# Kernel optimization log

Measured on AMD Instinct MI355X. Metric: run time of the kernel, lower is better.

Reference implementation:

```python
import jax, jax.numpy as jnp
import numpy as np
from jax import lax


def setup_inputs() -> dict:
    key = jax.random.key(0)
    k1, k2 = jax.random.split(key)
    x = jax.random.normal(k1, (16, 256, 64, 64), dtype=jnp.float32)
    weight = jax.random.normal(k2, (1024, 256), dtype=jnp.float32)  # codebook (K, C)
    return {"x": x, "weight": weight}


def reference(x, weight):
    B, C, H, W = x.shape
    # (b c h w) -> (b h w) c
    xf = jnp.transpose(x, (0, 2, 3, 1)).reshape(-1, C)  # [N, C]
    d = (jnp.sum(xf * xf, axis=1, keepdims=True)
         + jnp.sum(weight * weight, axis=1)
         - 2.0 * (xf @ weight.T))
    indices = jnp.argmin(d, axis=1)  # [N], int
    z = weight[indices]  # [N, C] embedding lookup
    codebook_loss = jnp.mean((z - lax.stop_gradient(xf)) ** 2)
    commitment_loss = jnp.mean((xf - lax.stop_gradient(z)) ** 2)
    # straight-through estimator
    zq = xf + lax.stop_gradient(z - xf)
    zq = zq.reshape(B, H, W, C).transpose(0, 3, 1, 2)  # back to [B, C, H, W]
    sequence = indices.reshape(B, H, W)
    return zq, sequence, codebook_loss, commitment_loss
```

## Files before the change

kernel.cpp:

```cpp
#include <hip/hip_runtime.h>
#include <cfloat>
#include <climits>

#define B_   16
#define C_   256
#define K_   1024
#define HW_  4096
#define N_   (B_ * HW_)
#define CHW_ (C_ * HW_)

#define SEQ_OFF  16777216
#define LOSS_OFF (SEQ_OFF + N_)
#define WT_F    0
#define WN_F    262144
#define WNU_F   263168
#define WQ_F    264192
#define RLIST_F 395264
#define RCNT_F  526336
#define WMAX_F  526337

#define RL_CAP  131072
#define EPS_GAP 0.1f
#define XSCL    20.0f
#define XINV    0.05f
#define XOVF    6.3f

typedef int i32x4 __attribute__((ext_vector_type(4)));

__device__ __forceinline__ int pack4b(int b0, int b1, int b2, int b3) {
    return (b0 & 0xFF) | ((b1 & 0xFF) << 8) | ((b2 & 0xFF) << 16) | ((b3 & 0xFF) << 24);
}

__global__ __launch_bounds__(256) void wmax_kernel(
    const float* __restrict__ w, unsigned* __restrict__ wmax_bits)
{
    const int tid = blockIdx.x * 256 + threadIdx.x;
    float mx = 0.f;
#pragma unroll
    for (int q = 0; q < 4; ++q) {
        const float4 v = reinterpret_cast<const float4*>(w)[tid * 4 + q];
        mx = fmaxf(mx, fmaxf(fmaxf(fabsf(v.x), fabsf(v.y)), fmaxf(fabsf(v.z), fabsf(v.w))));
    }
#pragma unroll
    for (int m = 1; m < 64; m <<= 1) mx = fmaxf(mx, __shfl_xor(mx, m, 64));
    if ((threadIdx.x & 63) == 0) atomicMax(wmax_bits, __float_as_uint(mx));
}

__global__ __launch_bounds__(256) void wprep_kernel(
    const float* __restrict__ w, const unsigned* __restrict__ wmax_bits,
    unsigned char* __restrict__ wq, float* __restrict__ w_t,
    float* __restrict__ wn, int* __restrict__ wnu)
{
    const int t = threadIdx.x;
    const int l = t & 63;
    const int k = blockIdx.x * 4 + (t >> 6);
    const float wmx = __uint_as_float(*wmax_bits);
    const float s   = 127.4f / wmx;
    const float d1  = wmx / 127.4f;
    const float sl  = s * 256.0f;

    const float4 v4 = *reinterpret_cast<const float4*>(w + (size_t)k * C_ + l * 4);
    float vv[4] = {v4.x, v4.y, v4.z, v4.w};
    float s2 = vv[0]*vv[0] + vv[1]*vv[1] + vv[2]*vv[2] + vv[3]*vv[3];
#pragma unroll
    for (int m = 1; m < 64; m <<= 1) s2 += __shfl_xor(s2, m, 64);

    const int chunk = k >> 4;
    const int col   = k & 15;
#pragma unroll
    for (int q = 0; q < 4; ++q) {
        const int c = l * 4 + q;
        const float v = vv[q];
        const int qh = (int)rintf(v * s);
        const float r = fmaf((float)qh, -d1, v);
        int ql = (int)rintf(r * sl);
        ql = max(-127, min(127, ql));
        const size_t off = (size_t)chunk * 8192 + (size_t)(c >> 6) * 1024
                         + (size_t)((c >> 4) & 3) * 256 + (size_t)col * 16 + (size_t)(c & 15);
        wq[off]        = (unsigned char)(qh & 0xFF);
        wq[off + 4096] = (unsigned char)(ql & 0xFF);
        w_t[(size_t)c * K_ + k] = v;
    }
    if (l == 0) {
        wn[k] = s2;
        wnu[k] = (int)rintf(s2 * (2560.0f / d1));
    }
}

__global__ __launch_bounds__(64, 2) void argmin_i8_kernel(
    const float* __restrict__ x, const unsigned char* __restrict__ wq,
    const int* __restrict__ wnu, const unsigned* __restrict__ wmax_bits,
    float* __restrict__ seq, int* __restrict__ rlist, int* __restrict__ rcount)
{
    const int l   = threadIdx.x;
    const int col = l & 15;
    const int kg  = l >> 4;
    const int nb  = blockIdx.x;
    const int b   = nb >> 7;
    const int hw0 = (nb & 127) << 5;
    const float* xb = x + (size_t)b * CHW_ + hw0;

    i32x4 ah[2][4], al[2][4];
    float mxr[2] = {0.f, 0.f};
#pragma unroll
    for (int t = 0; t < 2; ++t) {
        const int row = t * 16 + col;
#pragma unroll
        for (int s = 0; s < 4; ++s) {
            int qh[16], ql[16];
#pragma unroll
            for (int j = 0; j < 16; ++j) {
                const float v = xb[(size_t)(s * 64 + kg * 16 + j) * HW_ + row];
                mxr[t] = fmaxf(mxr[t], fabsf(v));
                int h = (int)rintf(v * XSCL);
                h = max(-127, min(127, h));
                const float r = fmaf((float)h, -XINV, v);
                int lo = (int)rintf(r * (XSCL * 256.0f));
                lo = max(-127, min(127, lo));
                qh[j] = h; ql[j] = lo;
            }
            ah[t][s] = (i32x4){ pack4b(qh[0],qh[1],qh[2],qh[3]),   pack4b(qh[4],qh[5],qh[6],qh[7]),
                                pack4b(qh[8],qh[9],qh[10],qh[11]), pack4b(qh[12],qh[13],qh[14],qh[15]) };
            al[t][s] = (i32x4){ pack4b(ql[0],ql[1],ql[2],ql[3]),   pack4b(ql[4],ql[5],ql[6],ql[7]),
                                pack4b(ql[8],ql[9],ql[10],ql[11]), pack4b(ql[12],ql[13],ql[14],ql[15]) };
        }
    }

#pragma unroll
    for (int t = 0; t < 2; ++t) {
        mxr[t] = fmaxf(mxr[t], __shfl_xor(mxr[t], 16, 64));
        mxr[t] = fmaxf(mxr[t], __shfl_xor(mxr[t], 32, 64));
        if (kg == 0 && mxr[t] > XOVF) {
            const int pos = atomicAdd(rcount, 1);
            if (pos < RL_CAP) rlist[pos] = b * HW_ + hw0 + t * 16 + col;
        }
    }

    const float wmx = __uint_as_float(*wmax_bits);
    const int eps_u = (int)(32614.4f / wmx);

    int m1p[2][4], m2p[2][4];
#pragma unroll
    for (int t = 0; t < 2; ++t)
#pragma unroll
        for (int i = 0; i < 4; ++i) { m1p[t][i] = INT_MAX; m2p[t][i] = INT_MAX; }

#pragma unroll 1
    for (int ch = 0; ch < 64; ++ch) {
        const unsigned char* base = wq + (size_t)ch * 8192 + l * 16;
        const int wnu_l = wnu[ch * 16 + col];

        i32x4 bh[4], bl[4];
#pragma unroll
        for (int s = 0; s < 4; ++s) {
            bh[s] = *reinterpret_cast<const i32x4*>(base + s * 1024);
            bl[s] = *reinterpret_cast<const i32x4*>(base + 4096 + s * 1024);
        }

        i32x4 aH0 = {0,0,0,0}, aH1 = {0,0,0,0};
        i32x4 aXa0 = {0,0,0,0}, aXb0 = {0,0,0,0};
        i32x4 aXa1 = {0,0,0,0}, aXb1 = {0,0,0,0};
#pragma unroll
        for (int s = 0; s < 4; ++s) {
            aH0  = __builtin_amdgcn_mfma_i32_16x16x64_i8(ah[0][s], bh[s], aH0, 0, 0, 0);
            aH1  = __builtin_amdgcn_mfma_i32_16x16x64_i8(ah[1][s], bh[s], aH1, 0, 0, 0);
            aXa0 = __builtin_amdgcn_mfma_i32_16x16x64_i8(ah[0][s], bl[s], aXa0, 0, 0, 0);
            aXb0 = __builtin_amdgcn_mfma_i32_16x16x64_i8(al[0][s], bh[s], aXb0, 0, 0, 0);
            aXa1 = __builtin_amdgcn_mfma_i32_16x16x64_i8(ah[1][s], bl[s], aXa1, 0, 0, 0);
            aXb1 = __builtin_amdgcn_mfma_i32_16x16x64_i8(al[1][s], bh[s], aXb1, 0, 0, 0);
        }

#pragma unroll
        for (int i = 0; i < 4; ++i) {
            const int T0  = (aH0[i] << 8) + aXa0[i] + aXb0[i];
            const int D0  = wnu_l - T0;
            const int Dp0 = (D0 & ~63) | ch;
            m2p[0][i] = min(m2p[0][i], max(m1p[0][i], Dp0));
            m1p[0][i] = min(m1p[0][i], Dp0);
            const int T1  = (aH1[i] << 8) + aXa1[i] + aXb1[i];
            const int D1  = wnu_l - T1;
            const int Dp1 = (D1 & ~63) | ch;
            m2p[1][i] = min(m2p[1][i], max(m1p[1][i], Dp1));
            m1p[1][i] = min(m1p[1][i], Dp1);
        }
    }

    int k1[2][4];
#pragma unroll
    for (int t = 0; t < 2; ++t)
#pragma unroll
        for (int i = 0; i < 4; ++i) k1[t][i] = ((m1p[t][i] & 63) << 4) | col;
#pragma unroll
    for (int mask = 1; mask <= 8; mask <<= 1) {
#pragma unroll
        for (int t = 0; t < 2; ++t) {
#pragma unroll
            for (int i = 0; i < 4; ++i) {
                const int om1 = __shfl_xor(m1p[t][i], mask, 64);
                const int ok1 = __shfl_xor(k1[t][i],  mask, 64);
                const int om2 = __shfl_xor(m2p[t][i], mask, 64);
                const int nm2 = min(min(m2p[t][i], om2), max(m1p[t][i], om1));
                const bool lt = om1 < m1p[t][i] || (om1 == m1p[t][i] && ok1 < k1[t][i]);
                m1p[t][i] = lt ? om1 : m1p[t][i];
                k1[t][i]  = lt ? ok1 : k1[t][i];
                m2p[t][i] = nm2;
            }
        }
    }

    if (col == 0) {
#pragma unroll
        for (int t = 0; t < 2; ++t) {
#pragma unroll
            for (int i = 0; i < 4; ++i) {
                const int row_local = t * 16 + kg * 4 + i;
                const int n = b * HW_ + hw0 + row_local;
                seq[n] = (float)k1[t][i];
                if (m2p[t][i] - m1p[t][i] < eps_u) {
                    const int pos = atomicAdd(rcount, 1);
                    if (pos < RL_CAP) rlist[pos] = n;
                }
            }
        }
    }
}

__global__ __launch_bounds__(256) void rescue_kernel(
    const float* __restrict__ x, const float* __restrict__ w_t,
    const float* __restrict__ wnorm, const int* __restrict__ rlist,
    const int* __restrict__ rcount, float* __restrict__ seq)
{
    __shared__ float xr[C_];
    __shared__ float bvs[4];
    __shared__ int   bis[4];
    const int t = threadIdx.x;
    const int cnt = min(*rcount, RL_CAP);
    for (int ii = blockIdx.x; ii < cnt; ii += gridDim.x) {
        const int n = rlist[ii];
        const int b = n >> 12, hw = n & 4095;
        xr[t] = x[(size_t)b * CHW_ + (size_t)t * HW_ + hw];
        __syncthreads();
        float best = FLT_MAX; int bidx = 0;
#pragma unroll
        for (int q = 0; q < 4; ++q) {
            const int k = t + q * 256;
            float acc = 0.f;
            for (int c = 0; c < C_; ++c) acc = fmaf(xr[c], w_t[(size_t)c * K_ + k], acc);
            const float d = wnorm[k] - 2.f * acc;
            if (d < best || (d == best && k < bidx)) { best = d; bidx = k; }
        }
#pragma unroll
        for (int mask = 1; mask < 64; mask <<= 1) {
            const float ov = __shfl_xor(best, mask, 64);
            const int   oi = __shfl_xor(bidx, mask, 64);
            if (ov < best || (ov == best && oi < bidx)) { best = ov; bidx = oi; }
        }
        if ((t & 63) == 0) { bvs[t >> 6] = best; bis[t >> 6] = bidx; }
        __syncthreads();
        if (t == 0) {
            float bv = bvs[0]; int bi = bis[0];
#pragma unroll
            for (int w2 = 1; w2 < 4; ++w2)
                if (bvs[w2] < bv || (bvs[w2] == bv && bis[w2] < bi)) { bv = bvs[w2]; bi = bis[w2]; }
            seq[n] = (float)bi;
        }
        __syncthreads();
    }
}

__global__ __launch_bounds__(256) void gather_kernel(
    const float* __restrict__ x, const float* __restrict__ w,
    const float* __restrict__ seqf, float* __restrict__ zq,
    double* __restrict__ loss_acc)
{
    __shared__ float ws[C_ * 64];
    const int t   = threadIdx.x;
    const int nb  = blockIdx.x;
    const int b   = nb >> 6;
    const int hw0 = (nb & 63) << 6;
    {
        const int j = t >> 2, q = t & 3;
        const int idx = (int)seqf[b * HW_ + hw0 + j];
        const float* wrow = w + (size_t)idx * C_ + q * 64;
#pragma unroll
        for (int m = 0; m < 16; ++m) {
            const float4 v = *reinterpret_cast<const float4*>(wrow + m * 4);
            const int c = q * 64 + m * 4;
            ws[(c + 0) * 64 + j] = v.x;
            ws[(c + 1) * 64 + j] = v.y;
            ws[(c + 2) * 64 + j] = v.z;
            ws[(c + 3) * 64 + j] = v.w;
        }
    }
    __syncthreads();
    const int r  = t & 63;
    const int cg = t >> 6;
    const float* xb = x  + (size_t)b * CHW_ + hw0;
    float*       zb = zq + (size_t)b * CHW_ + hw0;
    float lsum = 0.f;
#pragma unroll 4
    for (int cc = 0; cc < 64; ++cc) {
        const int c = cg * 64 + cc;
        const float xv = xb[(size_t)c * HW_ + r];
        const float d  = ws[c * 64 + r] - xv;
        zb[(size_t)c * HW_ + r] = xv + d;
        lsum += d * d;
    }
#pragma unroll
    for (int off = 32; off >= 1; off >>= 1) lsum += __shfl_down(lsum, off, 64);
    __syncthreads();
    if ((t & 63) == 0) ws[t >> 6] = lsum;
    __syncthreads();
    if (t == 0)
        atomicAdd(loss_acc, (double)(ws[0] + ws[1] + ws[2] + ws[3]));
}

__global__ void finalize_kernel(const double* __restrict__ acc, float* __restrict__ loss_out)
{
    const double s = *acc;
    const float m = (float)(s / (double)((size_t)N_ * C_));
    loss_out[0] = m;
    loss_out[1] = m;
}

extern "C" void kernel_launch(void* const* d_in, const int* in_sizes, int n_in,
                              void* d_out, int out_size, void* d_ws, size_t ws_size,
                              hipStream_t stream)
{
    (void)in_sizes; (void)n_in; (void)out_size; (void)d_ws; (void)ws_size;
    const float* x = (const float*)d_in[0];
    const float* w = (const float*)d_in[1];
    float* out = (float*)d_out;

    float*         w_t    = out + WT_F;
    float*         wn     = out + WN_F;
    int*           wnu    = (int*)(out + WNU_F);
    unsigned char* wq     = (unsigned char*)(out + WQ_F);
    int*           rlist  = (int*)(out + RLIST_F);
    int*           rcount = (int*)(out + RCNT_F);
    unsigned*      wmaxb  = (unsigned*)(out + WMAX_F);
    float*         seq    = out + SEQ_OFF;
    double*        loss_acc = (double*)(out + LOSS_OFF);

    hipMemsetAsync((void*)wmaxb, 0, 4, stream);
    hipMemsetAsync((void*)rcount, 0, 4, stream);
    wmax_kernel<<<64, 256, 0, stream>>>(w, wmaxb);
    wprep_kernel<<<256, 256, 0, stream>>>(w, wmaxb, wq, w_t, wn, wnu);
    argmin_i8_kernel<<<2048, 64, 0, stream>>>(x, wq, wnu, wmaxb, seq, rlist, rcount);
    rescue_kernel<<<1024, 256, 0, stream>>>(x, w_t, wn, rlist, rcount, seq);
    hipMemsetAsync((char*)d_out + (size_t)LOSS_OFF * 4, 0, 8, stream);
    gather_kernel<<<1024, 256, 0, stream>>>(x, w, seq, out, loss_acc);
    finalize_kernel<<<1, 1, 0, stream>>>(loss_acc, out + LOSS_OFF);
}
```

Before: 191.5 us.

## Split codebook across four blocks per row tile and merge partial top-2

The int8 MFMA argmin kernel now splits the 1024-entry codebook into four slices, one block per slice, so four times as many blocks run. Each block writes per-row partial (min, second-min) pairs with the full code index packed into the low 10 bits, and a new merge kernel combines them, writes the sequence and flags ambiguous rows for rescue. The inner loop double-buffers codebook register loads, and launch bounds are raised to allow more waves per SIMD. The costs are redundant quantisation of x in each of the four blocks, an extra kernel launch, and a partials buffer. The coarser distance mask is compensated by widening the rescue threshold, which may send more rows to the rescue kernel.

```diff
diff --git a/kernel.cpp b/kernel.cpp
--- a/kernel.cpp
+++ b/kernel.cpp
@@ -15,9 +15,10 @@
 #define WN_F    262144
 #define WNU_F   263168
 #define WQ_F    264192
-#define RLIST_F 395264
-#define RCNT_F  526336
-#define WMAX_F  526337
+#define PART_F  395264
+#define RLIST_F 919552
+#define RCNT_F  1050624
+#define WMAX_F  1050625
 
 #define RL_CAP  131072
 #define EPS_GAP 0.1f
@@ -87,17 +88,19 @@
     }
 }
 
-__global__ __launch_bounds__(64, 2) void argmin_i8_kernel(
+__global__ __launch_bounds__(64, 4) void argmin_i8_kernel(
     const float* __restrict__ x, const unsigned char* __restrict__ wq,
-    const int* __restrict__ wnu, const unsigned* __restrict__ wmax_bits,
-    float* __restrict__ seq, int* __restrict__ rlist, int* __restrict__ rcount)
+    const int* __restrict__ wnu, int2* __restrict__ part,
+    int* __restrict__ rlist, int* __restrict__ rcount)
 {
     const int l   = threadIdx.x;
     const int col = l & 15;
     const int kg  = l >> 4;
     const int nb  = blockIdx.x;
-    const int b   = nb >> 7;
-    const int hw0 = (nb & 127) << 5;
+    const int s   = nb & 3;
+    const int rb  = nb >> 2;
+    const int b   = rb >> 7;
+    const int hw0 = (rb & 127) << 5;
     const float* xb = x + (size_t)b * CHW_ + hw0;
 
     i32x4 ah[2][4], al[2][4];
@@ -106,11 +109,11 @@
     for (int t = 0; t < 2; ++t) {
         const int row = t * 16 + col;
 #pragma unroll
-        for (int s = 0; s < 4; ++s) {
+        for (int ss = 0; ss < 4; ++ss) {
             int qh[16], ql[16];
 #pragma unroll
             for (int j = 0; j < 16; ++j) {
-                const float v = xb[(size_t)(s * 64 + kg * 16 + j) * HW_ + row];
+                const float v = xb[(size_t)(ss * 64 + kg * 16 + j) * HW_ + row];
                 mxr[t] = fmaxf(mxr[t], fabsf(v));
                 int h = (int)rintf(v * XSCL);
                 h = max(-127, min(127, h));
@@ -119,25 +122,25 @@
                 lo = max(-127, min(127, lo));
                 qh[j] = h; ql[j] = lo;
             }
-            ah[t][s] = (i32x4){ pack4b(qh[0],qh[1],qh[2],qh[3]),   pack4b(qh[4],qh[5],qh[6],qh[7]),
-                                pack4b(qh[8],qh[9],qh[10],qh[11]), pack4b(qh[12],qh[13],qh[14],qh[15]) };
-            al[t][s] = (i32x4){ pack4b(ql[0],ql[1],ql[2],ql[3]),   pack4b(ql[4],ql[5],ql[6],ql[7]),
-                                pack4b(ql[8],ql[9],ql[10],ql[11]), pack4b(ql[12],ql[13],ql[14],ql[15]) };
-        }
-    }
-
-#pragma unroll
-    for (int t = 0; t < 2; ++t) {
-        mxr[t] = fmaxf(mxr[t], __shfl_xor(mxr[t], 16, 64));
-        mxr[t] = fmaxf(mxr[t], __shfl_xor(mxr[t], 32, 64));
-        if (kg == 0 && mxr[t] > XOVF) {
-            const int pos = atomicAdd(rcount, 1);
-            if (pos < RL_CAP) rlist[pos] = b * HW_ + hw0 + t * 16 + col;
-        }
-    }
-
-    const float wmx = __uint_as_float(*wmax_bits);
-    const int eps_u = (int)(32614.4f / wmx);
+            ah[t][ss] = (i32x4){ pack4b(qh[0],qh[1],qh[2],qh[3]),   pack4b(qh[4],qh[5],qh[6],qh[7]),
+                                 pack4b(qh[8],qh[9],qh[10],qh[11]), pack4b(qh[12],qh[13],qh[14],qh[15]) };
+            al[t][ss] = (i32x4){ pack4b(ql[0],ql[1],ql[2],ql[3]),   pack4b(ql[4],ql[5],ql[6],ql[7]),
+                                 pack4b(ql[8],ql[9],ql[10],ql[11]), pack4b(ql[12],ql[13],ql[14],ql[15]) };
+        }
+    }
+
+    if (s == 0) {
+#pragma unroll
+        for (int t = 0; t < 2; ++t) {
+            float m = mxr[t];
+            m = fmaxf(m, __shfl_xor(m, 16, 64));
+            m = fmaxf(m, __shfl_xor(m, 32, 64));
+            if (kg == 0 && m > XOVF) {
+                const int pos = atomicAdd(rcount, 1);
+                if (pos < RL_CAP) rlist[pos] = b * HW_ + hw0 + t * 16 + col;
+            }
+        }
+    }
 
     int m1p[2][4], m2p[2][4];
 #pragma unroll
@@ -145,51 +148,58 @@
 #pragma unroll
         for (int i = 0; i < 4; ++i) { m1p[t][i] = INT_MAX; m2p[t][i] = INT_MAX; }
 
+#define LOADB(gch, BH, BL)                                                        \
+    {                                                                             \
+        const unsigned char* base = wq + (size_t)(gch) * 8192 + l * 16;           \
+        _Pragma("unroll")                                                         \
+        for (int s4 = 0; s4 < 4; ++s4) {                                          \
+            BH[s4] = *reinterpret_cast<const i32x4*>(base + s4 * 1024);           \
+            BL[s4] = *reinterpret_cast<const i32x4*>(base + 4096 + s4 * 1024);    \
+        }                                                                         \
+    }
+
+#define COMPUTE(gch, BH, BL)                                                      \
+    {                                                                             \
+        const int wnu_l = wnu[(gch) * 16 + col];                                  \
+        i32x4 aH0 = {0,0,0,0}, aH1 = {0,0,0,0};                                   \
+        i32x4 aXa0 = {0,0,0,0}, aXb0 = {0,0,0,0};                                 \
+        i32x4 aXa1 = {0,0,0,0}, aXb1 = {0,0,0,0};                                 \
+        _Pragma("unroll")                                                         \
+        for (int s4 = 0; s4 < 4; ++s4) {                                          \
+            aH0  = __builtin_amdgcn_mfma_i32_16x16x64_i8(ah[0][s4], BH[s4], aH0, 0, 0, 0);  \
+            aH1  = __builtin_amdgcn_mfma_i32_16x16x64_i8(ah[1][s4], BH[s4], aH1, 0, 0, 0);  \
+            aXa0 = __builtin_amdgcn_mfma_i32_16x16x64_i8(ah[0][s4], BL[s4], aXa0, 0, 0, 0); \
+            aXb0 = __builtin_amdgcn_mfma_i32_16x16x64_i8(al[0][s4], BH[s4], aXb0, 0, 0, 0); \
+            aXa1 = __builtin_amdgcn_mfma_i32_16x16x64_i8(ah[1][s4], BL[s4], aXa1, 0, 0, 0); \
+            aXb1 = __builtin_amdgcn_mfma_i32_16x16x64_i8(al[1][s4], BH[s4], aXb1, 0, 0, 0); \
+        }                                                                         \
+        _Pragma("unroll")                                                         \
+        for (int i = 0; i < 4; ++i) {                                             \
+            const int T0  = (aH0[i] << 8) + aXa0[i] + aXb0[i];                    \
+            const int Dp0 = ((wnu_l - T0) & ~1023) | (((gch) << 4) | col);        \
+            m2p[0][i] = min(m2p[0][i], max(m1p[0][i], Dp0));                      \
+            m1p[0][i] = min(m1p[0][i], Dp0);                                      \
+            const int T1  = (aH1[i] << 8) + aXa1[i] + aXb1[i];                    \
+            const int Dp1 = ((wnu_l - T1) & ~1023) | (((gch) << 4) | col);        \
+            m2p[1][i] = min(m2p[1][i], max(m1p[1][i], Dp1));                      \
+            m1p[1][i] = min(m1p[1][i], Dp1);                                      \
+        }                                                                         \
+    }
+
+    i32x4 bha[4], bla[4], bhb[4], blb[4];
+    const int ch0 = s * 16;
+    LOADB(ch0, bha, bla);
 #pragma unroll 1
-    for (int ch = 0; ch < 64; ++ch) {
-        const unsigned char* base = wq + (size_t)ch * 8192 + l * 16;
-        const int wnu_l = wnu[ch * 16 + col];
-
-        i32x4 bh[4], bl[4];
-#pragma unroll
-        for (int s = 0; s < 4; ++s) {
-            bh[s] = *reinterpret_cast<const i32x4*>(base + s * 1024);
-            bl[s] = *reinterpret_cast<const i32x4*>(base + 4096 + s * 1024);
-        }
-
-        i32x4 aH0 = {0,0,0,0}, aH1 = {0,0,0,0};
-        i32x4 aXa0 = {0,0,0,0}, aXb0 = {0,0,0,0};
-        i32x4 aXa1 = {0,0,0,0}, aXb1 = {0,0,0,0};
-#pragma unroll
-        for (int s = 0; s < 4; ++s) {
-            aH0  = __builtin_amdgcn_mfma_i32_16x16x64_i8(ah[0][s], bh[s], aH0, 0, 0, 0);
-            aH1  = __builtin_amdgcn_mfma_i32_16x16x64_i8(ah[1][s], bh[s], aH1, 0, 0, 0);
-            aXa0 = __builtin_amdgcn_mfma_i32_16x16x64_i8(ah[0][s], bl[s], aXa0, 0, 0, 0);
-            aXb0 = __builtin_amdgcn_mfma_i32_16x16x64_i8(al[0][s], bh[s], aXb0, 0, 0, 0);
-            aXa1 = __builtin_amdgcn_mfma_i32_16x16x64_i8(ah[1][s], bl[s], aXa1, 0, 0, 0);
-            aXb1 = __builtin_amdgcn_mfma_i32_16x16x64_i8(al[1][s], bh[s], aXb1, 0, 0, 0);
-        }
-
-#pragma unroll
-        for (int i = 0; i < 4; ++i) {
-            const int T0  = (aH0[i] << 8) + aXa0[i] + aXb0[i];
-            const int D0  = wnu_l - T0;
-            const int Dp0 = (D0 & ~63) | ch;
-            m2p[0][i] = min(m2p[0][i], max(m1p[0][i], Dp0));
-            m1p[0][i] = min(m1p[0][i], Dp0);
-            const int T1  = (aH1[i] << 8) + aXa1[i] + aXb1[i];
-            const int D1  = wnu_l - T1;
-            const int Dp1 = (D1 & ~63) | ch;
-            m2p[1][i] = min(m2p[1][i], max(m1p[1][i], Dp1));
-            m1p[1][i] = min(m1p[1][i], Dp1);
-        }
-    }
-
-    int k1[2][4];
-#pragma unroll
-    for (int t = 0; t < 2; ++t)
-#pragma unroll
-        for (int i = 0; i < 4; ++i) k1[t][i] = ((m1p[t][i] & 63) << 4) | col;
+    for (int c2 = 0; c2 < 8; ++c2) {
+        const int e = ch0 + c2 * 2;
+        LOADB(e + 1, bhb, blb);
+        COMPUTE(e, bha, bla);
+        if (c2 < 7) LOADB(e + 2, bha, bla);
+        COMPUTE(e + 1, bhb, blb);
+    }
+#undef LOADB
+#undef COMPUTE
+
 #pragma unroll
     for (int mask = 1; mask <= 8; mask <<= 1) {
 #pragma unroll
@@ -197,12 +207,9 @@
 #pragma unroll
             for (int i = 0; i < 4; ++i) {
                 const int om1 = __shfl_xor(m1p[t][i], mask, 64);
-                const int ok1 = __shfl_xor(k1[t][i],  mask, 64);
                 const int om2 = __shfl_xor(m2p[t][i], mask, 64);
                 const int nm2 = min(min(m2p[t][i], om2), max(m1p[t][i], om1));
-                const bool lt = om1 < m1p[t][i] || (om1 == m1p[t][i] && ok1 < k1[t][i]);
-                m1p[t][i] = lt ? om1 : m1p[t][i];
-                k1[t][i]  = lt ? ok1 : k1[t][i];
+                m1p[t][i] = min(m1p[t][i], om1);
                 m2p[t][i] = nm2;
             }
         }
@@ -213,15 +220,33 @@
         for (int t = 0; t < 2; ++t) {
 #pragma unroll
             for (int i = 0; i < 4; ++i) {
-                const int row_local = t * 16 + kg * 4 + i;
-                const int n = b * HW_ + hw0 + row_local;
-                seq[n] = (float)k1[t][i];
-                if (m2p[t][i] - m1p[t][i] < eps_u) {
-                    const int pos = atomicAdd(rcount, 1);
-                    if (pos < RL_CAP) rlist[pos] = n;
-                }
+                const int n = b * HW_ + hw0 + t * 16 + kg * 4 + i;
+                part[((size_t)n << 2) | s] = make_int2(m1p[t][i], m2p[t][i]);
             }
         }
+    }
+}
+
+__global__ __launch_bounds__(256) void merge_kernel(
+    const int2* __restrict__ part, const unsigned* __restrict__ wmax_bits,
+    float* __restrict__ seq, int* __restrict__ rlist, int* __restrict__ rcount)
+{
+    const int n = blockIdx.x * 256 + threadIdx.x;
+    const int2* p = part + ((size_t)n << 2);
+    int m1 = INT_MAX, m2 = INT_MAX;
+#pragma unroll
+    for (int s = 0; s < 4; ++s) {
+        const int2 v = p[s];
+        m2 = min(m2, max(m1, v.x));
+        m1 = min(m1, v.x);
+        m2 = min(m2, v.y);
+    }
+    seq[n] = (float)(m1 & 1023);
+    const float wmx = __uint_as_float(*wmax_bits);
+    const int eps_u = (int)(32614.4f / wmx) + 1024;
+    if (m2 - m1 < eps_u) {
+        const int pos = atomicAdd(rcount, 1);
+        if (pos < RL_CAP) rlist[pos] = n;
     }
 }
 
@@ -336,6 +361,7 @@
     float*         wn     = out + WN_F;
     int*           wnu    = (int*)(out + WNU_F);
     unsigned char* wq     = (unsigned char*)(out + WQ_F);
+    int2*          part   = (int2*)(out + PART_F);
     int*           rlist  = (int*)(out + RLIST_F);
     int*           rcount = (int*)(out + RCNT_F);
     unsigned*      wmaxb  = (unsigned*)(out + WMAX_F);
@@ -346,7 +372,8 @@
     hipMemsetAsync((void*)rcount, 0, 4, stream);
     wmax_kernel<<<64, 256, 0, stream>>>(w, wmaxb);
     wprep_kernel<<<256, 256, 0, stream>>>(w, wmaxb, wq, w_t, wn, wnu);
-    argmin_i8_kernel<<<2048, 64, 0, stream>>>(x, wq, wnu, wmaxb, seq, rlist, rcount);
+    argmin_i8_kernel<<<8192, 64, 0, stream>>>(x, wq, wnu, part, rlist, rcount);
+    merge_kernel<<<256, 256, 0, stream>>>(part, wmaxb, seq, rlist, rcount);
     rescue_kernel<<<1024, 256, 0, stream>>>(x, w_t, wn, rlist, rcount, seq);
     hipMemsetAsync((char*)d_out + (size_t)LOSS_OFF * 4, 0, 8, stream);
     gather_kernel<<<1024, 256, 0, stream>>>(x, w, seq, out, loss_acc);
```

Measured after the change: 475.8 us. 2.48x slower.
